# Optimization experiments

Hardware: AMD Instinct MI355X
Metric: run time of the kernel (lower is better)

## Reference

```python
import jax, jax.numpy as jnp
import numpy as np

IMG_SIZE = np.array([960.0, 512.0], np.float32)   # network input size (w, h)
HM_SIZE = np.array([480.0, 256.0], np.float32)    # heatmap size = IMG_SIZE / 2 (w, h)
GRID_SIZE = np.array([8000.0, 8000.0, 2000.0], np.float32)  # mm
CUBE = (80, 80, 20)
NBINS = CUBE[0] * CUBE[1] * CUBE[2]


def _base_grid():
    # linspace(-size/2, size/2, nbins) per axis, meshgrid indexing='ij' (torch default)
    axes = [np.linspace(-GRID_SIZE[d] / 2, GRID_SIZE[d] / 2, CUBE[d], dtype=np.float32) for d in range(3)]
    gx, gy, gz = np.meshgrid(*axes, indexing='ij')
    return jnp.asarray(np.stack([gx.ravel(), gy.ravel(), gz.ravel()], axis=1))  # [NBINS, 3]


def _bilinear_sample(img, coords):
    # img: [C,H,W]; coords: [P,2] normalized to [-1,1], align_corners=True, zero padding
    C, H, W = img.shape
    ix = (coords[:, 0] + 1.0) * 0.5 * (W - 1)
    iy = (coords[:, 1] + 1.0) * 0.5 * (H - 1)
    x0 = jnp.floor(ix)
    y0 = jnp.floor(iy)
    x1 = x0 + 1.0
    y1 = y0 + 1.0
    wx1 = ix - x0
    wx0 = 1.0 - wx1
    wy1 = iy - y0
    wy0 = 1.0 - wy1

    def corner(xi, yi, w):
        valid = (xi >= 0) & (xi <= W - 1) & (yi >= 0) & (yi <= H - 1)
        xc = jnp.clip(xi, 0, W - 1).astype(jnp.int32)
        yc = jnp.clip(yi, 0, H - 1).astype(jnp.int32)
        vals = img[:, yc, xc]  # [C,P]
        return vals * (w * valid.astype(img.dtype))[None, :]

    return (corner(x0, y0, wx0 * wy0) + corner(x1, y0, wx1 * wy0)
            + corner(x0, y1, wx0 * wy1) + corner(x1, y1, wx1 * wy1))  # [C,P]


def reference(heatmaps, R, T, f, c_cam, trans, wh, grid_center):
    # heatmaps: [N,B,C,H,W]; R:[N,B,3,3]; T:[N,B,3]; f,c_cam,wh:[N,B,2]; trans:[N,B,2,3]; grid_center:[B,3]
    N, B, C, H, W = heatmaps.shape
    hm = jnp.asarray(HM_SIZE)
    img_sz = jnp.asarray(IMG_SIZE)

    grids = _base_grid()[None, :, :] + grid_center[:, None, :]          # [B,P,3]
    pts = grids[None, :, :, :] - T[:, :, None, :]                        # [N,B,P,3]
    xcam = jnp.einsum('nbij,nbpj->nbpi', R, pts)                         # [N,B,P,3]
    xy = f[:, :, None, :] * (xcam[..., :2] / xcam[..., 2:3]) + c_cam[:, :, None, :]  # pixel coords

    bnd = jnp.all((xy >= 0) & (xy < wh[:, :, None, :]), axis=-1).astype(heatmaps.dtype)  # [N,B,P]

    mx = jnp.max(wh, axis=-1)[:, :, None, None]
    xy = jnp.minimum(jnp.maximum(xy, -1.0), mx)
    xy1 = jnp.concatenate([xy, jnp.ones_like(xy[..., :1])], axis=-1)     # homogeneous
    xy = jnp.einsum('nbij,nbpj->nbpi', trans, xy1)                       # affine to network image space
    xy = xy * (hm / img_sz)
    sg = jnp.clip(xy / (hm - 1.0) * 2.0 - 1.0, -1.1, 1.1)                # [N,B,P,2]

    samples = jax.vmap(_bilinear_sample)(
        heatmaps.reshape(N * B, C, H, W), sg.reshape(N * B, NBINS, 2)
    ).reshape(N, B, C, NBINS)                                            # [N,B,C,P]

    bnd_e = bnd[:, :, None, :]                                           # [N,B,1,P]
    cubes = jnp.sum(samples * bnd_e, axis=0) / (jnp.sum(bnd_e, axis=0) + 1e-6)  # [B,C,P]
    cubes = jnp.nan_to_num(cubes)
    cubes = jnp.clip(cubes, 0.0, 1.0)  # feature_op = False
    cubes = cubes.reshape(B, C, CUBE[0], CUBE[1], CUBE[2])
    return cubes, grids


def setup_inputs():
    key = jax.random.key(0)
    k_hm, k_gc = jax.random.split(key)
    N, B, C, H, W = 5, 8, 15, 256, 480
    heatmaps = jax.random.uniform(k_hm, (N, B, C, H, W), jnp.float32)

    # plausible look-at cameras around the space center
    center = np.array([0.0, -500.0, 800.0], np.float32)
    Rs, Ts = [], []
    for i in range(N):
        ang = 2.0 * np.pi * i / N
        pos = center + np.array([6000.0 * np.cos(ang), 6000.0 * np.sin(ang), 1200.0], np.float32)
        fwd = center - pos
        fwd = fwd / np.linalg.norm(fwd)
        up = np.array([0.0, 0.0, 1.0], np.float32)
        right = np.cross(fwd, up)
        right = right / np.linalg.norm(right)
        down = np.cross(fwd, right)
        Rs.append(np.stack([right, down, fwd]).astype(np.float32))
        Ts.append(pos)
    R = jnp.asarray(np.broadcast_to(np.stack(Rs)[:, None], (N, B, 3, 3)).copy())
    T = jnp.asarray(np.broadcast_to(np.stack(Ts)[:, None], (N, B, 3)).copy())
    f = jnp.full((N, B, 2), 1500.0, jnp.float32)
    wh_np = np.array([1920.0, 1080.0], np.float32)  # original image width/height
    c_cam = jnp.asarray(np.broadcast_to(wh_np / 2, (N, B, 2)).copy())
    s = IMG_SIZE / wh_np
    tr = np.array([[s[0], 0.0, 0.0], [0.0, s[1], 0.0]], np.float32)
    trans = jnp.asarray(np.broadcast_to(tr, (N, B, 2, 3)).copy())
    wh = jnp.asarray(np.broadcast_to(wh_np, (N, B, 2)).copy())
    grid_center = jnp.asarray(center)[None, :] + 200.0 * jax.random.normal(k_gc, (B, 3), jnp.float32)
    return dict(heatmaps=heatmaps, R=R, T=T, f=f, c_cam=c_cam, trans=trans, wh=wh, grid_center=grid_center)
```

## Files before the change

### kernel.cpp

```cpp
#include <hip/hip_runtime.h>
#include <stdint.h>

#define N_VIEWS 5
#define B_ 8
#define C_ 15
#define CP_ 16
#define H_ 256
#define W_ 480
#define NBINS 128000
#define HW_ (H_ * W_)
#define CUBES_ELEMS (B_ * C_ * NBINS)
#define NB_ (N_VIEWS * B_)

typedef float v2f __attribute__((ext_vector_type(2)));

__global__ __launch_bounds__(256) void transpose_fp8_kernel(
    const float* __restrict__ hm, uint32_t* __restrict__ tp)
{
    const int bid  = blockIdx.x;
    const int b    = bid & 7;
    const int rest = bid >> 3;
    const int n    = rest % 5;
    const int tile = rest / 5;
    const int cb   = n * B_ + b;
    const int idx  = tile * 256 + (int)threadIdx.x;
    if (idx >= HW_) return;
    const float* src = hm + (size_t)cb * C_ * HW_ + idx;
    float v[CP_];
#pragma unroll
    for (int c = 0; c < C_; ++c) v[c] = src[(size_t)c * HW_];
    v[15] = 0.0f;
    uint32_t w[4];
#pragma unroll
    for (int j = 0; j < 4; ++j) {
        int r = 0;
        r = __builtin_amdgcn_cvt_pk_fp8_f32(v[4*j + 0], v[4*j + 1], r, false);
        r = __builtin_amdgcn_cvt_pk_fp8_f32(v[4*j + 2], v[4*j + 3], r, true);
        w[j] = (uint32_t)r;
    }
    uint4* dst = (uint4*)(tp + ((size_t)cb * HW_ + (size_t)idx) * 4);
    *dst = make_uint4(w[0], w[1], w[2], w[3]);
}

struct Proj { int o00, o10, o01, o11; float w00, w10, w01, w11, inb; };

__device__ __forceinline__ Proj project_one(
    int cb, float gx, float gy, float gz,
    const float* __restrict__ R, const float* __restrict__ T,
    const float* __restrict__ f, const float* __restrict__ ccam,
    const float* __restrict__ trans, const float* __restrict__ wh)
{
    Proj r;
    const float* Rn = R + cb * 9;
    const float px = gx - T[cb * 3 + 0];
    const float py = gy - T[cb * 3 + 1];
    const float pz = gz - T[cb * 3 + 2];
    const float xcm = Rn[0] * px + Rn[1] * py + Rn[2] * pz;
    const float ycm = Rn[3] * px + Rn[4] * py + Rn[5] * pz;
    const float zcm = Rn[6] * px + Rn[7] * py + Rn[8] * pz;
    const float u = f[cb * 2 + 0] * (xcm / zcm) + ccam[cb * 2 + 0];
    const float v = f[cb * 2 + 1] * (ycm / zcm) + ccam[cb * 2 + 1];
    const float w0 = wh[cb * 2 + 0], w1 = wh[cb * 2 + 1];
    const bool inb = (u >= 0.0f) & (u < w0) & (v >= 0.0f) & (v < w1);
    const float inbf = inb ? 1.0f : 0.0f;
    const float mx = fmaxf(w0, w1);
    const float uu = fminf(fmaxf(u, -1.0f), mx);
    const float vv = fminf(fmaxf(v, -1.0f), mx);
    const float* tr = trans + cb * 6;
    const float tx = (tr[0] * uu + tr[1] * vv + tr[2]) * 0.5f;
    const float ty = (tr[3] * uu + tr[4] * vv + tr[5]) * 0.5f;
    const float sgx = fminf(fmaxf(tx / 479.0f * 2.0f - 1.0f, -1.1f), 1.1f);
    const float sgy = fminf(fmaxf(ty / 255.0f * 2.0f - 1.0f, -1.1f), 1.1f);
    const float ixf = (sgx + 1.0f) * 0.5f * 479.0f;
    const float iyf = (sgy + 1.0f) * 0.5f * 255.0f;
    const float x0 = floorf(ixf), y0 = floorf(iyf);
    const float x1 = x0 + 1.0f, y1 = y0 + 1.0f;
    const float wx1 = ixf - x0, wy1 = iyf - y0;
    const float wx0 = 1.0f - wx1, wy0 = 1.0f - wy1;
    const float v00 = (x0 >= 0.0f && y0 >= 0.0f) ? inbf : 0.0f;
    const float v10 = (x1 <= 479.0f && y0 >= 0.0f) ? inbf : 0.0f;
    const float v01 = (x0 >= 0.0f && y1 <= 255.0f) ? inbf : 0.0f;
    const float v11 = (x1 <= 479.0f && y1 <= 255.0f) ? inbf : 0.0f;
    r.w00 = wx0 * wy0 * v00; r.w10 = wx1 * wy0 * v10;
    r.w01 = wx0 * wy1 * v01; r.w11 = wx1 * wy1 * v11;
    const int xi0 = min(max((int)x0, 0), W_ - 1);
    const int yi0 = min(max((int)y0, 0), H_ - 1);
    const int xi1 = min(max((int)x1, 0), W_ - 1);
    const int yi1 = min(max((int)y1, 0), H_ - 1);
    const int o00 = yi0 * W_ + xi0, o10 = yi0 * W_ + xi1;
    const int o01 = yi1 * W_ + xi0, o11 = yi1 * W_ + xi1;
    r.o00 = inb ? o00 : 0; r.o10 = inb ? o10 : 0;
    r.o01 = inb ? o01 : 0; r.o11 = inb ? o11 : 0;
    r.inb = inbf;
    return r;
}

__device__ __forceinline__ void decode_grid(int p, int b, const float* __restrict__ gc,
                                            float& gx, float& gy, float& gz)
{
    const int ixg = p / 1600;
    const int rem = p - ixg * 1600;
    const int iyg = rem / 20;
    const int izg = rem - iyg * 20;
    gx = (float)(-4000.0 + ixg * (8000.0 / 79.0)) + gc[b * 3 + 0];
    gy = (float)(-4000.0 + iyg * (8000.0 / 79.0)) + gc[b * 3 + 1];
    gz = (float)(-1000.0 + izg * (2000.0 / 19.0)) + gc[b * 3 + 2];
}

__device__ __forceinline__ void acc_pixel(float* acc, uint4 q, float wgt)
{
    const uint32_t u[4] = { q.x, q.y, q.z, q.w };
#pragma unroll
    for (int j = 0; j < 4; ++j) {
        v2f lo = __builtin_amdgcn_cvt_pk_f32_fp8(u[j], false);
        v2f hi = __builtin_amdgcn_cvt_pk_f32_fp8(u[j], true);
        acc[4*j + 0] += wgt * lo.x;
        acc[4*j + 1] += wgt * lo.y;
        acc[4*j + 2] += wgt * hi.x;
        acc[4*j + 3] += wgt * hi.y;
    }
}

__global__ __launch_bounds__(256) void project_kernel_fp8(
    const uint32_t* __restrict__ tp,
    const float* __restrict__ R, const float* __restrict__ T,
    const float* __restrict__ f, const float* __restrict__ ccam,
    const float* __restrict__ trans, const float* __restrict__ wh,
    const float* __restrict__ gc,
    float* __restrict__ out)
{
    const int bid = blockIdx.x;
    const int b   = bid & 7;
    const int p   = (bid >> 3) * 256 + (int)threadIdx.x;
    if (p >= NBINS) return;

    float gx, gy, gz;
    decode_grid(p, b, gc, gx, gy, gz);
    {
        const size_t goff = (size_t)CUBES_ELEMS + ((size_t)b * NBINS + (size_t)p) * 3;
        out[goff + 0] = gx; out[goff + 1] = gy; out[goff + 2] = gz;
    }

    Proj pr[N_VIEWS];
    uint4 q[N_VIEWS][4];
#pragma unroll
    for (int n = 0; n < N_VIEWS; ++n) {
        const int cb = n * B_ + b;
        pr[n] = project_one(cb, gx, gy, gz, R, T, f, ccam, trans, wh);
        const uint4* base = (const uint4*)tp + (size_t)cb * HW_;
        if (__any(pr[n].inb != 0.0f)) {
            q[n][0] = base[pr[n].o00];
            q[n][1] = base[pr[n].o10];
            q[n][2] = base[pr[n].o01];
            q[n][3] = base[pr[n].o11];
        } else {
            q[n][0] = q[n][1] = q[n][2] = q[n][3] = make_uint4(0u, 0u, 0u, 0u);
        }
    }

    float acc[CP_];
#pragma unroll
    for (int c = 0; c < CP_; ++c) acc[c] = 0.0f;
    float bndsum = 0.0f;
#pragma unroll
    for (int n = 0; n < N_VIEWS; ++n) {
        bndsum += pr[n].inb;
        acc_pixel(acc, q[n][0], pr[n].w00);
        acc_pixel(acc, q[n][1], pr[n].w10);
        acc_pixel(acc, q[n][2], pr[n].w01);
        acc_pixel(acc, q[n][3], pr[n].w11);
    }

    const float inv = 1.0f / (bndsum + 1e-6f);
    const size_t ob = (size_t)b * C_ * NBINS + (size_t)p;
#pragma unroll
    for (int c = 0; c < C_; ++c) {
        float r = acc[c] * inv;
        r = fmaxf(r, 0.0f);
        r = fminf(r, 1.0f);
        out[ob + (size_t)c * NBINS] = r;
    }
}

__global__ __launch_bounds__(256) void project_kernel_direct(
    const float* __restrict__ hm,
    const float* __restrict__ R, const float* __restrict__ T,
    const float* __restrict__ f, const float* __restrict__ ccam,
    const float* __restrict__ trans, const float* __restrict__ wh,
    const float* __restrict__ gc,
    float* __restrict__ out)
{
    const int p = blockIdx.x * blockDim.x + threadIdx.x;
    const int b = blockIdx.y;
    if (p >= NBINS) return;
    float gx, gy, gz;
    decode_grid(p, b, gc, gx, gy, gz);
    {
        const size_t goff = (size_t)CUBES_ELEMS + ((size_t)b * NBINS + (size_t)p) * 3;
        out[goff + 0] = gx; out[goff + 1] = gy; out[goff + 2] = gz;
    }
    float acc[C_];
#pragma unroll
    for (int c = 0; c < C_; ++c) acc[c] = 0.0f;
    float bndsum = 0.0f;
#pragma unroll
    for (int n = 0; n < N_VIEWS; ++n) {
        const int cb = n * B_ + b;
        Proj cr = project_one(cb, gx, gy, gz, R, T, f, ccam, trans, wh);
        bndsum += cr.inb;
        const float* img = hm + (size_t)cb * C_ * HW_;
#pragma unroll
        for (int c = 0; c < C_; ++c) {
            const float* ic = img + (size_t)c * HW_;
            acc[c] += cr.w00 * ic[cr.o00] + cr.w10 * ic[cr.o10]
                    + cr.w01 * ic[cr.o01] + cr.w11 * ic[cr.o11];
        }
    }
    const float inv = 1.0f / (bndsum + 1e-6f);
    const size_t ob = (size_t)b * C_ * NBINS + (size_t)p;
#pragma unroll
    for (int c = 0; c < C_; ++c) {
        float r = acc[c] * inv;
        r = fmaxf(r, 0.0f);
        r = fminf(r, 1.0f);
        out[ob + (size_t)c * NBINS] = r;
    }
}

extern "C" void kernel_launch(void* const* d_in, const int* in_sizes, int n_in,
                              void* d_out, int out_size, void* d_ws, size_t ws_size,
                              hipStream_t stream) {
    const float* hm    = (const float*)d_in[0];
    const float* R     = (const float*)d_in[1];
    const float* T     = (const float*)d_in[2];
    const float* f     = (const float*)d_in[3];
    const float* ccam  = (const float*)d_in[4];
    const float* trans = (const float*)d_in[5];
    const float* wh    = (const float*)d_in[6];
    const float* gc    = (const float*)d_in[7];
    float* out = (float*)d_out;

    const size_t ws_needed = (size_t)NB_ * HW_ * CP_;

    if (ws_size >= ws_needed) {
        uint32_t* tp = (uint32_t*)d_ws;
        dim3 tgrid((HW_ / 256) * NB_);
        transpose_fp8_kernel<<<tgrid, 256, 0, stream>>>(hm, tp);
        dim3 grid((NBINS / 256) * B_);
        project_kernel_fp8<<<grid, 256, 0, stream>>>(tp, R, T, f, ccam, trans, wh, gc, out);
    } else {
        dim3 grid(NBINS / 256, B_);
        project_kernel_direct<<<grid, 256, 0, stream>>>(hm, R, T, f, ccam, trans, wh, gc, out);
    }
}
```

Before: 484.0 us.

## Split projection views across wavefronts and reduce channel sums in shared memory

Each block now handles 64 grid points with 5 wavefronts, one per camera view, instead of one thread looping over all views. Per-view accumulators go to padded LDS and are reduced after a barrier, then written out channel by channel. This is meant to cut per-thread register pressure and the serial gather latency so more memory requests are in flight. The cost is an LDS round trip, a __syncthreads per block, and four times as many blocks. The early skip of fetches for views with no in-bounds lanes is also removed, so those wavefronts always issue their loads.

```diff
diff --git a/kernel.cpp b/kernel.cpp
--- a/kernel.cpp
+++ b/kernel.cpp
@@ -121,7 +121,7 @@
     }
 }
 
-__global__ __launch_bounds__(256) void project_kernel_fp8(
+__global__ __launch_bounds__(320) void project_kernel_fp8(
     const uint32_t* __restrict__ tp,
     const float* __restrict__ R, const float* __restrict__ T,
     const float* __restrict__ f, const float* __restrict__ ccam,
@@ -129,56 +129,62 @@
     const float* __restrict__ gc,
     float* __restrict__ out)
 {
-    const int bid = blockIdx.x;
-    const int b   = bid & 7;
-    const int p   = (bid >> 3) * 256 + (int)threadIdx.x;
-    if (p >= NBINS) return;
+    __shared__ float s_acc[N_VIEWS][64 * 17];
+    __shared__ float s_inb[N_VIEWS][64];
+
+    const int bid  = blockIdx.x;
+    const int b    = bid & 7;
+    const int p0   = (bid >> 3) * 64;
+    const int tid  = (int)threadIdx.x;
+    const int lane = tid & 63;
+    const int view = tid >> 6;
+    const int p    = p0 + lane;
+    const int cb   = view * B_ + b;
 
     float gx, gy, gz;
     decode_grid(p, b, gc, gx, gy, gz);
-    {
+    if (view == 0) {
         const size_t goff = (size_t)CUBES_ELEMS + ((size_t)b * NBINS + (size_t)p) * 3;
         out[goff + 0] = gx; out[goff + 1] = gy; out[goff + 2] = gz;
     }
 
-    Proj pr[N_VIEWS];
-    uint4 q[N_VIEWS][4];
-#pragma unroll
-    for (int n = 0; n < N_VIEWS; ++n) {
-        const int cb = n * B_ + b;
-        pr[n] = project_one(cb, gx, gy, gz, R, T, f, ccam, trans, wh);
-        const uint4* base = (const uint4*)tp + (size_t)cb * HW_;
-        if (__any(pr[n].inb != 0.0f)) {
-            q[n][0] = base[pr[n].o00];
-            q[n][1] = base[pr[n].o10];
-            q[n][2] = base[pr[n].o01];
-            q[n][3] = base[pr[n].o11];
-        } else {
-            q[n][0] = q[n][1] = q[n][2] = q[n][3] = make_uint4(0u, 0u, 0u, 0u);
+    const Proj pr = project_one(cb, gx, gy, gz, R, T, f, ccam, trans, wh);
+    const uint4* base = (const uint4*)tp + (size_t)cb * HW_;
+    const uint4 q00 = base[pr.o00];
+    const uint4 q10 = base[pr.o10];
+    const uint4 q01 = base[pr.o01];
+    const uint4 q11 = base[pr.o11];
+
+    float acc[CP_];
+#pragma unroll
+    for (int c = 0; c < CP_; ++c) acc[c] = 0.0f;
+    acc_pixel(acc, q00, pr.w00);
+    acc_pixel(acc, q10, pr.w10);
+    acc_pixel(acc, q01, pr.w01);
+    acc_pixel(acc, q11, pr.w11);
+
+    float* dst = &s_acc[view][lane * 17];
+#pragma unroll
+    for (int c = 0; c < CP_; ++c) dst[c] = acc[c];
+    s_inb[view][lane] = pr.inb;
+    __syncthreads();
+
+#pragma unroll
+    for (int item = tid; item < 1024; item += 320) {
+        const int ch = item >> 6;
+        const int pt = item & 63;
+        if (ch < C_) {
+            float s = 0.0f, bnd = 0.0f;
+#pragma unroll
+            for (int v = 0; v < N_VIEWS; ++v) {
+                s   += s_acc[v][pt * 17 + ch];
+                bnd += s_inb[v][pt];
+            }
+            float r = s * (1.0f / (bnd + 1e-6f));
+            r = fmaxf(r, 0.0f);
+            r = fminf(r, 1.0f);
+            out[(size_t)b * C_ * NBINS + (size_t)ch * NBINS + (size_t)(p0 + pt)] = r;
         }
-    }
-
-    float acc[CP_];
-#pragma unroll
-    for (int c = 0; c < CP_; ++c) acc[c] = 0.0f;
-    float bndsum = 0.0f;
-#pragma unroll
-    for (int n = 0; n < N_VIEWS; ++n) {
-        bndsum += pr[n].inb;
-        acc_pixel(acc, q[n][0], pr[n].w00);
-        acc_pixel(acc, q[n][1], pr[n].w10);
-        acc_pixel(acc, q[n][2], pr[n].w01);
-        acc_pixel(acc, q[n][3], pr[n].w11);
-    }
-
-    const float inv = 1.0f / (bndsum + 1e-6f);
-    const size_t ob = (size_t)b * C_ * NBINS + (size_t)p;
-#pragma unroll
-    for (int c = 0; c < C_; ++c) {
-        float r = acc[c] * inv;
-        r = fmaxf(r, 0.0f);
-        r = fminf(r, 1.0f);
-        out[ob + (size_t)c * NBINS] = r;
     }
 }
 
@@ -246,8 +252,8 @@
         uint32_t* tp = (uint32_t*)d_ws;
         dim3 tgrid((HW_ / 256) * NB_);
         transpose_fp8_kernel<<<tgrid, 256, 0, stream>>>(hm, tp);
-        dim3 grid((NBINS / 256) * B_);
-        project_kernel_fp8<<<grid, 256, 0, stream>>>(tp, R, T, f, ccam, trans, wh, gc, out);
+        dim3 grid((NBINS / 64) * B_);
+        project_kernel_fp8<<<grid, 320, 0, stream>>>(tp, R, T, f, ccam, trans, wh, gc, out);
     } else {
         dim3 grid(NBINS / 256, B_);
         project_kernel_direct<<<grid, 256, 0, stream>>>(hm, R, T, f, ccam, trans, wh, gc, out);
```

Result: slower. 500.7 us (+3.4%).
